# Performance work log

Hardware: AMD Instinct MI355X
Metric: run time of the kernel (lower is better)

## Reference

```python
import jax, jax.numpy as jnp
import numpy as np

B, S, D_MODEL, N_HEADS = 4, 2048, 1024, 16
HEAD_DIM = D_MODEL // N_HEADS  # 64; used only for the softmax scale, as in the source


def setup_inputs() -> dict:
    key = jax.random.key(0)
    kq, kk, kv, kw = jax.random.split(key, 4)
    q = jax.random.normal(kq, (B, S, D_MODEL), dtype=jnp.float32)
    k = jax.random.normal(kk, (B, S, D_MODEL), dtype=jnp.float32)
    v = jax.random.normal(kv, (B, S, D_MODEL), dtype=jnp.float32)
    # out_proj: nn.Linear(d_model, d_model, bias=False) -> weight [out, in]
    W_out = jax.random.normal(kw, (D_MODEL, D_MODEL), dtype=jnp.float32) * (1.0 / np.sqrt(D_MODEL))
    return {"q": q, "k": k, "v": v, "W_out": W_out}


def reference(q, k, v, W_out):
    scale = 1.0 / jnp.sqrt(jnp.float32(HEAD_DIM))
    # scores: [B, Sq, Sk] -- full quadratic score matrix, as in the source
    scores = jnp.einsum("bqd,bkd->bqk", q, k) * scale
    attn = jax.nn.softmax(scores, axis=-1)
    out = jnp.einsum("bqk,bkd->bqd", attn, v)
    # torch Linear: y = x @ W^T
    return jnp.einsum("bsd,ed->bse", out, W_out)
```

## Files before the change

kernel.cpp:

```cpp
#include <hip/hip_runtime.h>
#include <hip/hip_fp16.h>
#include <stdint.h>

typedef _Float16 h16;
typedef _Float16 h16x8 __attribute__((ext_vector_type(8)));
typedef float f32x4 __attribute__((ext_vector_type(4)));

#define BB 4
#define SS 2048
#define DD 1024

__device__ __forceinline__ void gload16(const void* g, void* l) {
    __builtin_amdgcn_global_load_lds(
        (const __attribute__((address_space(1))) uint32_t*)g,
        (__attribute__((address_space(3))) uint32_t*)l, 16, 0, 0);
}

__global__ __launch_bounds__(256) void cvt_all(
    const float* __restrict__ q, const float* __restrict__ k,
    const float* __restrict__ v, const float* __restrict__ w,
    h16* __restrict__ qh, h16* __restrict__ kh,
    h16* __restrict__ vh, h16* __restrict__ wh) {
    int b = blockIdx.x;
    const float* src; h16* dst; float sc = 1.0f;
    if (b < 2048)      { src = q; dst = qh; sc = 0.125f; }
    else if (b < 4096) { src = k; dst = kh; b -= 2048; }
    else if (b < 6144) { src = v; dst = vh; b -= 4096; }
    else               { src = w; dst = wh; b -= 6144; }
    size_t base = (size_t)b * 1024 + threadIdx.x;
#pragma unroll
    for (int i = 0; i < 4; ++i) {
        size_t g = base + (size_t)i * 256;
        float4 a = ((const float4*)src)[g];
        union { int2 i2; h16 h[4]; } u;
        u.h[0] = (h16)(a.x * sc); u.h[1] = (h16)(a.y * sc);
        u.h[2] = (h16)(a.z * sc); u.h[3] = (h16)(a.w * sc);
        ((int2*)dst)[g] = u.i2;
    }
}

template<bool F32OUT>
__global__ __launch_bounds__(256, 2) void gemm2p_sm(
    const h16* __restrict__ A, const h16* __restrict__ B, void* __restrict__ Cv,
    int lda, int ldb, int ldc, int K, int tilesN, int tilesMN,
    long long aBatch, long long bBatch, long long cBatch)
{
    constexpr int ABYTES = 128 * 128;
    constexpr int BBYTES = 128 * 128;
    constexpr int BUFB   = ABYTES + BBYTES;

    __shared__ __align__(1024) char lds[2 * BUFB];

    const int tid = threadIdx.x;
    const int nwg = gridDim.x;
    const int bid = blockIdx.x;
    const int wgid = (bid & 7) * (nwg >> 3) + (bid >> 3);
    const int bb  = wgid / tilesMN;
    const int rem = wgid % tilesMN;
    const int tm = rem / tilesN, tn = rem % tilesN;
    const int row0 = tm * 128, col0 = tn * 128;

    const h16* Ab = A + (long long)bb * aBatch;
    const h16* Bb = B + (long long)bb * bBatch;

    const int lane = tid & 63, wid = tid >> 6;
    const int wm = wid >> 1, wn = wid & 1;
    const int frow = lane & 15, kq = lane >> 4;

    const int NT = K >> 6;

    f32x4 acc[4][4];
#pragma unroll
    for (int m = 0; m < 4; ++m)
#pragma unroll
        for (int n = 0; n < 4; ++n) acc[m][n] = (f32x4){0.f, 0.f, 0.f, 0.f};

    char* l0 = (char*)lds;

    auto STAGE_B = [&](int kt, int buf) {
#pragma unroll
        for (int i = 0; i < 4; ++i) {
            int d = i * 256 + tid;
            int s = d & 7, r = d >> 3;
            int gg = s ^ (r & 7);
            gload16(Bb + (size_t)(col0 + r) * ldb + kt + gg * 8,
                    l0 + buf * BUFB + ABYTES + (r * 8 + s) * 16);
        }
    };
    auto STAGE_AH = [&](int kt, int buf, int mh) {
#pragma unroll
        for (int i = 0; i < 2; ++i) {
            int d = i * 256 + tid;
            int s = d & 7, hr = d >> 3;
            int r = ((hr & ~31) << 1) + mh * 32 + (hr & 31);
            int gg = s ^ (r & 7);
            gload16(Ab + (size_t)(row0 + r) * lda + kt + gg * 8,
                    l0 + buf * BUFB + (r * 8 + s) * 16);
        }
    };
    auto READ_A = [&](int buf, int mh, h16x8 (&af)[2][2]) {
#pragma unroll
        for (int mm = 0; mm < 2; ++mm)
#pragma unroll
            for (int ks = 0; ks < 2; ++ks) {
                int r = wm * 64 + (mh * 2 + mm) * 16 + frow;
                int s = (ks * 4 + kq) ^ (r & 7);
                af[mm][ks] = *(const h16x8*)(l0 + buf * BUFB + (r * 8 + s) * 16);
            }
    };
    auto READ_B = [&](int buf, h16x8 (&bf)[4][2]) {
#pragma unroll
        for (int nn = 0; nn < 4; ++nn)
#pragma unroll
            for (int ks = 0; ks < 2; ++ks) {
                int r = wn * 64 + nn * 16 + frow;
                int s = (ks * 4 + kq) ^ (r & 7);
                bf[nn][ks] = *(const h16x8*)(l0 + buf * BUFB + ABYTES + (r * 8 + s) * 16);
            }
    };
    auto MFMA_H = [&](int mh, h16x8 (&af)[2][2], h16x8 (&bf)[4][2]) {
        __builtin_amdgcn_s_setprio(1);
#pragma unroll
        for (int ks = 0; ks < 2; ++ks)
#pragma unroll
            for (int mm = 0; mm < 2; ++mm)
#pragma unroll
                for (int nn = 0; nn < 4; ++nn)
                    acc[mh * 2 + mm][nn] =
                        __builtin_amdgcn_mfma_f32_16x16x32_f16(
                            af[mm][ks], bf[nn][ks], acc[mh * 2 + mm][nn], 0, 0, 0);
        __builtin_amdgcn_s_setprio(0);
    };

    STAGE_B(0, 0); STAGE_AH(0, 0, 0); STAGE_AH(0, 0, 1);
    asm volatile("s_waitcnt vmcnt(2)" ::: "memory");
    __builtin_amdgcn_s_barrier();

    h16x8 af[2][2], bf[4][2];

    for (int G = 0; G < NT; ++G) {
        const int buf = G & 1;
        const int kt1 = (G + 1) << 6;
        if (G + 1 < NT) {
            STAGE_B(kt1, buf ^ 1);
            STAGE_AH(kt1, buf ^ 1, 0);
            STAGE_AH(kt1, buf ^ 1, 1);
        }
        READ_A(buf, 0, af);
        READ_B(buf, bf);
        MFMA_H(0, af, bf);
        if (G + 1 < NT) asm volatile("s_waitcnt vmcnt(8)" ::: "memory");
        else            asm volatile("s_waitcnt vmcnt(0)" ::: "memory");
        __builtin_amdgcn_s_barrier();
        READ_A(buf, 1, af);
        MFMA_H(1, af, bf);
        if (G + 1 >= NT) break;
        asm volatile("s_waitcnt vmcnt(2)" ::: "memory");
        __builtin_amdgcn_s_barrier();
    }

    const int erow = row0 + wm * 64 + (lane >> 4) * 4;
    const int ecol = col0 + wn * 64 + (lane & 15);
    if (F32OUT) {
        float* C = (float*)Cv + (long long)bb * cBatch;
#pragma unroll
        for (int m = 0; m < 4; ++m)
#pragma unroll
            for (int n = 0; n < 4; ++n)
#pragma unroll
                for (int j = 0; j < 4; ++j)
                    C[(size_t)(erow + m * 16 + j) * ldc + (ecol + n * 16)] = acc[m][n][j];
    } else {
        h16* C = (h16*)Cv + (long long)bb * cBatch;
#pragma unroll
        for (int m = 0; m < 4; ++m)
#pragma unroll
            for (int n = 0; n < 4; ++n)
#pragma unroll
                for (int j = 0; j < 4; ++j)
                    C[(size_t)(erow + m * 16 + j) * ldc + (ecol + n * 16)] = (h16)acc[m][n][j];
    }
}

__global__ __launch_bounds__(256) void softmax_rows(h16* __restrict__ buf) {
    const int row = blockIdx.x;
    h16* rp = buf + (size_t)row * 2048;
    const int t = threadIdx.x;
    const int lane = t & 63, wid = t >> 6;

    union { int4 i4; h16 h[8]; } u;
    u.i4 = ((const int4*)rp)[t];
    float f[8];
#pragma unroll
    for (int j = 0; j < 8; ++j) f[j] = (float)u.h[j];

    float m = f[0];
#pragma unroll
    for (int j = 1; j < 8; ++j) m = fmaxf(m, f[j]);
#pragma unroll
    for (int off = 32; off; off >>= 1) m = fmaxf(m, __shfl_xor(m, off));

    __shared__ float smax[4];
    __shared__ float ssum[4];
    if (lane == 0) smax[wid] = m;
    __syncthreads();
    m = fmaxf(fmaxf(smax[0], smax[1]), fmaxf(smax[2], smax[3]));

    float s = 0.f;
#pragma unroll
    for (int j = 0; j < 8; ++j) { f[j] = __expf(f[j] - m); s += f[j]; }
#pragma unroll
    for (int off = 32; off; off >>= 1) s += __shfl_xor(s, off);
    if (lane == 0) ssum[wid] = s;
    __syncthreads();
    float inv = 1.0f / (ssum[0] + ssum[1] + ssum[2] + ssum[3]);

#pragma unroll
    for (int j = 0; j < 8; ++j) u.h[j] = (h16)(f[j] * inv);
    ((int4*)rp)[t] = u.i4;
}

extern "C" void kernel_launch(void* const* d_in, const int* in_sizes, int n_in,
                              void* d_out, int out_size, void* d_ws, size_t ws_size,
                              hipStream_t stream) {
    (void)in_sizes; (void)n_in; (void)out_size; (void)ws_size;
    const float* q = (const float*)d_in[0];
    const float* k = (const float*)d_in[1];
    const float* v = (const float*)d_in[2];
    const float* w = (const float*)d_in[3];
    float* out = (float*)d_out;

    const size_t QKV = (size_t)BB * SS * DD;
    h16* qh = (h16*)d_ws;
    h16* kh = qh + QKV;
    h16* vh = kh + QKV;
    h16* wh = vh + QKV;
    h16* sc = wh + (size_t)DD * DD;

    cvt_all<<<6400, 256, 0, stream>>>(q, k, v, w, qh, kh, vh, wh);

    gemm2p_sm<false><<<1024, 256, 0, stream>>>(
        qh, kh, (void*)sc, DD, DD, SS, DD, 16, 256,
        (long long)SS * DD, (long long)SS * DD, (long long)SS * SS);

    softmax_rows<<<BB * SS, 256, 0, stream>>>(sc);

    h16* vpT = qh;
    gemm2p_sm<false><<<512, 256, 0, stream>>>(
        wh, vh, (void*)vpT, DD, DD, BB * SS, DD, 64, 512,
        0LL, 0LL, 0LL);

    gemm2p_sm<true><<<512, 256, 0, stream>>>(
        sc, vpT, (void*)out, SS, BB * SS, DD, SS, 8, 128,
        (long long)SS * SS, (long long)SS, (long long)SS * DD);
}
```

Baseline: 144.7 us.

## Fuse fp32-to-fp16 conversion into GEMM tile loading, drop separate convert pass

Removes the standalone conversion kernel that wrote fp16 copies of q, k, v and W to workspace. The QK^T and W·V^T GEMMs now load fp32 tiles into registers, convert them to fp16 and store them into swizzled LDS inside the GEMM. The softmax scale moves to the output epilogue. This saves a full read-and-write pass over the inputs, but the GEMM main loop now uses register-staged loads, a full vmcnt(0) wait and two barriers per k-step instead of async direct-to-LDS loads, which can cut overlap and raise register pressure.

```diff
diff --git a/kernel.cpp b/kernel.cpp
--- a/kernel.cpp
+++ b/kernel.cpp
@@ -16,26 +16,145 @@
         (__attribute__((address_space(3))) uint32_t*)l, 16, 0, 0);
 }
 
-__global__ __launch_bounds__(256) void cvt_all(
-    const float* __restrict__ q, const float* __restrict__ k,
-    const float* __restrict__ v, const float* __restrict__ w,
-    h16* __restrict__ qh, h16* __restrict__ kh,
-    h16* __restrict__ vh, h16* __restrict__ wh) {
-    int b = blockIdx.x;
-    const float* src; h16* dst; float sc = 1.0f;
-    if (b < 2048)      { src = q; dst = qh; sc = 0.125f; }
-    else if (b < 4096) { src = k; dst = kh; b -= 2048; }
-    else if (b < 6144) { src = v; dst = vh; b -= 4096; }
-    else               { src = w; dst = wh; b -= 6144; }
-    size_t base = (size_t)b * 1024 + threadIdx.x;
-#pragma unroll
-    for (int i = 0; i < 4; ++i) {
-        size_t g = base + (size_t)i * 256;
-        float4 a = ((const float4*)src)[g];
-        union { int2 i2; h16 h[4]; } u;
-        u.h[0] = (h16)(a.x * sc); u.h[1] = (h16)(a.y * sc);
-        u.h[2] = (h16)(a.z * sc); u.h[3] = (h16)(a.w * sc);
-        ((int2*)dst)[g] = u.i2;
+template<bool F32OUT>
+__global__ __launch_bounds__(256, 2) void gemm_f32(
+    const float* __restrict__ A, const float* __restrict__ B, void* __restrict__ Cv,
+    int lda, int ldb, int ldc, int K, int tilesN, int tilesMN,
+    long long aBatch, long long bBatch, long long cBatch, float oscale)
+{
+    constexpr int ABYTES = 128 * 128;
+    constexpr int BUFB   = 2 * ABYTES;
+
+    __shared__ __align__(1024) char lds[2 * BUFB];
+
+    const int tid = threadIdx.x;
+    const int nwg = gridDim.x;
+    const int bid = blockIdx.x;
+    const int wgid = (bid & 7) * (nwg >> 3) + (bid >> 3);
+    const int bb  = wgid / tilesMN;
+    const int rem = wgid % tilesMN;
+    const int tm = rem / tilesN, tn = rem % tilesN;
+    const int row0 = tm * 128, col0 = tn * 128;
+
+    const float* Ab = A + (long long)bb * aBatch;
+    const float* Bb = B + (long long)bb * bBatch;
+
+    const int lane = tid & 63, wid = tid >> 6;
+    const int wm = wid >> 1, wn = wid & 1;
+    const int frow = lane & 15, kq = lane >> 4;
+    const int rr = tid >> 3, gg = tid & 7;
+
+    const int NT = K >> 6;
+
+    f32x4 acc[4][4];
+#pragma unroll
+    for (int m = 0; m < 4; ++m)
+#pragma unroll
+        for (int n = 0; n < 4; ++n) acc[m][n] = (f32x4){0.f, 0.f, 0.f, 0.f};
+
+    char* l0 = (char*)lds;
+
+    float4 la[8], lb[8];
+    auto LOADS = [&](int kt) {
+#pragma unroll
+        for (int p = 0; p < 4; ++p) {
+            int r = p * 32 + rr;
+            const float* pa = Ab + (size_t)(row0 + r) * lda + kt + gg * 8;
+            la[2 * p]     = *(const float4*)pa;
+            la[2 * p + 1] = *(const float4*)(pa + 4);
+            const float* pb = Bb + (size_t)(col0 + r) * ldb + kt + gg * 8;
+            lb[2 * p]     = *(const float4*)pb;
+            lb[2 * p + 1] = *(const float4*)(pb + 4);
+        }
+    };
+    auto CVTWRITE = [&](int buf) {
+#pragma unroll
+        for (int p = 0; p < 4; ++p) {
+            int r = p * 32 + rr;
+            int s = gg ^ (r & 7);
+            union { int4 i4; h16 h[8]; } ua, ub;
+            float4 x = la[2 * p], y = la[2 * p + 1];
+            ua.h[0] = (h16)x.x; ua.h[1] = (h16)x.y; ua.h[2] = (h16)x.z; ua.h[3] = (h16)x.w;
+            ua.h[4] = (h16)y.x; ua.h[5] = (h16)y.y; ua.h[6] = (h16)y.z; ua.h[7] = (h16)y.w;
+            x = lb[2 * p]; y = lb[2 * p + 1];
+            ub.h[0] = (h16)x.x; ub.h[1] = (h16)x.y; ub.h[2] = (h16)x.z; ub.h[3] = (h16)x.w;
+            ub.h[4] = (h16)y.x; ub.h[5] = (h16)y.y; ub.h[6] = (h16)y.z; ub.h[7] = (h16)y.w;
+            *(int4*)(l0 + buf * BUFB + (r * 8 + s) * 16) = ua.i4;
+            *(int4*)(l0 + buf * BUFB + ABYTES + (r * 8 + s) * 16) = ub.i4;
+        }
+    };
+    auto READ_A = [&](int buf, h16x8 (&af)[4][2]) {
+#pragma unroll
+        for (int mm = 0; mm < 4; ++mm)
+#pragma unroll
+            for (int ks = 0; ks < 2; ++ks) {
+                int r = wm * 64 + mm * 16 + frow;
+                int s = (ks * 4 + kq) ^ (r & 7);
+                af[mm][ks] = *(const h16x8*)(l0 + buf * BUFB + (r * 8 + s) * 16);
+            }
+    };
+    auto READ_B = [&](int buf, h16x8 (&bf)[4][2]) {
+#pragma unroll
+        for (int nn = 0; nn < 4; ++nn)
+#pragma unroll
+            for (int ks = 0; ks < 2; ++ks) {
+                int r = wn * 64 + nn * 16 + frow;
+                int s = (ks * 4 + kq) ^ (r & 7);
+                bf[nn][ks] = *(const h16x8*)(l0 + buf * BUFB + ABYTES + (r * 8 + s) * 16);
+            }
+    };
+
+    LOADS(0);
+    asm volatile("s_waitcnt vmcnt(0)" ::: "memory");
+    CVTWRITE(0);
+    asm volatile("s_waitcnt lgkmcnt(0)" ::: "memory");
+    __builtin_amdgcn_s_barrier();
+
+    for (int G = 0; G < NT; ++G) {
+        const int bufR = G & 1;
+        if (G + 1 < NT) LOADS((G + 1) << 6);
+        h16x8 af[4][2], bf[4][2];
+        READ_A(bufR, af);
+        READ_B(bufR, bf);
+        __builtin_amdgcn_s_setprio(1);
+#pragma unroll
+        for (int ks = 0; ks < 2; ++ks)
+#pragma unroll
+            for (int mm = 0; mm < 4; ++mm)
+#pragma unroll
+                for (int nn = 0; nn < 4; ++nn)
+                    acc[mm][nn] = __builtin_amdgcn_mfma_f32_16x16x32_f16(
+                        af[mm][ks], bf[nn][ks], acc[mm][nn], 0, 0, 0);
+        __builtin_amdgcn_s_setprio(0);
+        if (G + 1 < NT) {
+            asm volatile("s_waitcnt vmcnt(0) lgkmcnt(0)" ::: "memory");
+            __builtin_amdgcn_s_barrier();
+            CVTWRITE(bufR ^ 1);
+            asm volatile("s_waitcnt lgkmcnt(0)" ::: "memory");
+            __builtin_amdgcn_s_barrier();
+        }
+    }
+
+    const int erow = row0 + wm * 64 + (lane >> 4) * 4;
+    const int ecol = col0 + wn * 64 + (lane & 15);
+    if (F32OUT) {
+        float* C = (float*)Cv + (long long)bb * cBatch;
+#pragma unroll
+        for (int m = 0; m < 4; ++m)
+#pragma unroll
+            for (int n = 0; n < 4; ++n)
+#pragma unroll
+                for (int j = 0; j < 4; ++j)
+                    C[(size_t)(erow + m * 16 + j) * ldc + (ecol + n * 16)] = acc[m][n][j] * oscale;
+    } else {
+        h16* C = (h16*)Cv + (long long)bb * cBatch;
+#pragma unroll
+        for (int m = 0; m < 4; ++m)
+#pragma unroll
+            for (int n = 0; n < 4; ++n)
+#pragma unroll
+                for (int j = 0; j < 4; ++j)
+                    C[(size_t)(erow + m * 16 + j) * ldc + (ecol + n * 16)] = (h16)(acc[m][n][j] * oscale);
     }
 }
 
@@ -230,25 +349,18 @@
     const float* w = (const float*)d_in[3];
     float* out = (float*)d_out;
 
-    const size_t QKV = (size_t)BB * SS * DD;
-    h16* qh = (h16*)d_ws;
-    h16* kh = qh + QKV;
-    h16* vh = kh + QKV;
-    h16* wh = vh + QKV;
-    h16* sc = wh + (size_t)DD * DD;
-
-    cvt_all<<<6400, 256, 0, stream>>>(q, k, v, w, qh, kh, vh, wh);
-
-    gemm2p_sm<false><<<1024, 256, 0, stream>>>(
-        qh, kh, (void*)sc, DD, DD, SS, DD, 16, 256,
-        (long long)SS * DD, (long long)SS * DD, (long long)SS * SS);
+    h16* vpT = (h16*)d_ws;
+    h16* sc  = vpT + (size_t)DD * BB * SS;
+
+    gemm_f32<false><<<1024, 256, 0, stream>>>(
+        q, k, (void*)sc, DD, DD, SS, DD, 16, 256,
+        (long long)SS * DD, (long long)SS * DD, (long long)SS * SS, 0.125f);
 
     softmax_rows<<<BB * SS, 256, 0, stream>>>(sc);
 
-    h16* vpT = qh;
-    gemm2p_sm<false><<<512, 256, 0, stream>>>(
-        wh, vh, (void*)vpT, DD, DD, BB * SS, DD, 64, 512,
-        0LL, 0LL, 0LL);
+    gemm_f32<false><<<512, 256, 0, stream>>>(
+        w, v, (void*)vpT, DD, DD, BB * SS, DD, 64, 512,
+        0LL, 0LL, 0LL, 1.0f);
 
     gemm2p_sm<true><<<512, 256, 0, stream>>>(
         sc, vpT, (void*)out, SS, BB * SS, DD, SS, 8, 128,
```

Measured after the change: 164.2 us. +13.5%, slower.
